# Optimization experiments

Hardware: AMD Instinct MI355X
Metric: run time of the kernel (lower is better)

## Reference

```python
import jax, jax.numpy as jnp
import numpy as np

B, L, D, H, DF = 256, 96, 512, 8, 2048
HD = D // H
SCALE = HD ** (-0.5)  # scale param (lsa=False -> constant)
EPS = 1e-5


def layer_norm(x, g, b):
    m = jnp.mean(x, axis=-1, keepdims=True)
    v = jnp.mean((x - m) ** 2, axis=-1, keepdims=True)
    return (x - m) * jax.lax.rsqrt(v + EPS) * g + b


def setup_inputs() -> dict:
    key = jax.random.key(0)
    ks = jax.random.split(key, 16)
    w = lambda k, shape: jax.random.normal(k, shape, jnp.float32) * 0.02
    return {
        "src": jax.random.normal(ks[0], (B, L, D), jnp.float32),
        "Wq": w(ks[1], (D, D)), "bq": jnp.zeros((D,), jnp.float32),
        "Wk": w(ks[2], (D, D)), "bk": jnp.zeros((D,), jnp.float32),
        "Wv": w(ks[3], (D, D)), "bv": jnp.zeros((D,), jnp.float32),
        "matrix": jax.random.normal(ks[4], (B, H, L, L), jnp.float32),  # learned per-(batch,head) score matrix
        "Wo": w(ks[5], (D, D)), "bo": jnp.zeros((D,), jnp.float32),
        "ln1_g": jnp.ones((D,), jnp.float32), "ln1_b": jnp.zeros((D,), jnp.float32),
        "W1": w(ks[6], (D, DF)), "b1": jnp.zeros((DF,), jnp.float32),
        "W2": w(ks[7], (DF, D)), "b2": jnp.zeros((D,), jnp.float32),
        "ln2_g": jnp.ones((D,), jnp.float32), "ln2_b": jnp.zeros((D,), jnp.float32),
    }


def reference(src, Wq, bq, Wk, bk, Wv, bv, matrix, Wo, bo,
              ln1_g, ln1_b, W1, b1, W2, b2, ln2_g, ln2_b):
    # --- multi-head attention with custom elementwise score matrix (NFIC=1) ---
    q = (src @ Wq + bq).reshape(B, L, H, HD).transpose(0, 2, 1, 3)  # [B,H,L,hd]
    k = (src @ Wk + bk).reshape(B, L, H, HD).transpose(0, 2, 1, 3)
    v = (src @ Wv + bv).reshape(B, L, H, HD).transpose(0, 2, 1, 3)
    scores = jnp.einsum("bhqd,bhkd->bhqk", q, k) * matrix * SCALE  # [B,H,L,L]
    attn = jax.nn.softmax(scores, axis=-1)
    out = jnp.einsum("bhqk,bhkd->bhqd", attn, v)  # [B,H,L,hd]
    out = out.transpose(0, 2, 1, 3).reshape(B, L, D) @ Wo + bo
    # --- residual + norm (post-norm) ---
    x = layer_norm(src + out, ln1_g, ln1_b)
    # --- FFN ---
    ff = jax.nn.gelu(x @ W1 + b1, approximate=False) @ W2 + b2
    y = layer_norm(x + ff, ln2_g, ln2_b)
    return (y, scores)
```

## Files before the change

kernel.cpp:

```cpp
#include <hip/hip_runtime.h>
#include <hip/hip_bf16.h>
#include <math.h>

typedef __attribute__((ext_vector_type(8))) short short8;
typedef __attribute__((ext_vector_type(4))) float floatx4;

__device__ __forceinline__ void load_lds16(const void* g, void* l) {
  __builtin_amdgcn_global_load_lds(
      (__attribute__((address_space(1))) void*)(g),
      (__attribute__((address_space(3))) void*)(l), 16, 0, 0);
}

#define MFMA16x16x32(a, b, c) __builtin_amdgcn_mfma_f32_16x16x32_bf16((a), (b), (c), 0, 0, 0)

__device__ __forceinline__ float to_f(float x) { return x; }
__device__ __forceinline__ float to_f(__hip_bfloat16 x) { return __bfloat162float(x); }
__device__ __forceinline__ void st_val(float* p, float v) { *p = v; }
__device__ __forceinline__ void st_val(__hip_bfloat16* p, float v) { *p = __float2bfloat16(v); }

__global__ __launch_bounds__(256) void cvt_f32_bf16(const float4* __restrict__ in,
                                                    ushort* __restrict__ out) {
  int i = blockIdx.x * 256 + threadIdx.x;
  float4 v = in[i];
  ushort4 o;
  __hip_bfloat16 b0 = __float2bfloat16(v.x);
  __hip_bfloat16 b1 = __float2bfloat16(v.y);
  __hip_bfloat16 b2 = __float2bfloat16(v.z);
  __hip_bfloat16 b3 = __float2bfloat16(v.w);
  o.x = *(ushort*)&b0; o.y = *(ushort*)&b1; o.z = *(ushort*)&b2; o.w = *(ushort*)&b3;
  *(ushort4*)(out + 4 * i) = o;
}

__global__ void concat3(const float* __restrict__ a, const float* __restrict__ b,
                        const float* __restrict__ c, float* __restrict__ o) {
  int i = blockIdx.x * 256 + threadIdx.x;
  o[i] = i < 512 ? a[i] : (i < 1024 ? b[i - 512] : c[i - 1024]);
}

__global__ void transpose_cvt(const float* __restrict__ in,
                              __hip_bfloat16* __restrict__ out, int R, int C) {
  __shared__ __hip_bfloat16 tile[32][33];
  int bx = blockIdx.x * 32, by = blockIdx.y * 32;
  int tx = threadIdx.x, ty = threadIdx.y;
  for (int i = ty; i < 32; i += 8)
    tile[i][tx] = __float2bfloat16(in[(size_t)(by + i) * C + bx + tx]);
  __syncthreads();
  for (int i = ty; i < 32; i += 8) out[(size_t)(bx + i) * R + by + tx] = tile[tx][i];
}

__global__ __launch_bounds__(256, 3) void gemm128(
    const __hip_bfloat16* __restrict__ A,
    const __hip_bfloat16* __restrict__ BT,
    const float* __restrict__ bias,
    __hip_bfloat16* __restrict__ C,
    int N, int K, int act, int tiles_x) {
  __shared__ __align__(16) short8 smv[2048];
  char* smc = (char*)smv;
  const int tid = threadIdx.x;
  const int wave = tid >> 6, lane = tid & 63;
  const int quad = lane >> 4, m = lane & 15;
  const int wmi = wave >> 1, wni = wave & 1;
  const int nwg = gridDim.x;
  const int wg = (blockIdx.x & 7) * (nwg >> 3) + (blockIdx.x >> 3);
  const int row0 = (wg / tiles_x) * 128;
  const int col0 = (wg % tiles_x) * 128;
  const int nt = K >> 6;

  const int colb = (((lane & 7) ^ (lane >> 3)) << 4);
  const int rbase = wave * 8 + (lane >> 3);
  const char* pA[4];
  const char* pB[4];
  char* dA[4];
  char* dB[4];
#pragma unroll
  for (int r = 0; r < 4; ++r) {
    pA[r] = (const char*)(A + (size_t)(row0 + rbase + r * 32) * K) + colb;
    pB[r] = (const char*)(BT + (size_t)(col0 + rbase + r * 32) * K) + colb;
    dA[r] = smc + (r * 4 + wave) * 1024;
    dB[r] = smc + 16384 + (r * 4 + wave) * 1024;
  }

  const int rc0 = m * 8 + ((quad)     ^ (m & 7));
  const int rc1 = m * 8 + ((quad + 4) ^ (m & 7));
  const int aB = wmi * 512;
  const int bB = 1024 + wni * 512;

  floatx4 acc[4][4] = {};

  for (int t = 0; t < nt; ++t) {
#pragma unroll
    for (int r = 0; r < 4; ++r) { load_lds16(pA[r], dA[r]); pA[r] += 128; }
#pragma unroll
    for (int r = 0; r < 4; ++r) { load_lds16(pB[r], dB[r]); pB[r] += 128; }
    __syncthreads();
    short8 aF[4], bF[4];
#pragma unroll
    for (int i = 0; i < 4; ++i) aF[i] = smv[aB + i * 128 + rc0];
#pragma unroll
    for (int j = 0; j < 4; ++j) bF[j] = smv[bB + j * 128 + rc0];
#pragma unroll
    for (int i = 0; i < 4; ++i)
#pragma unroll
      for (int j = 0; j < 4; ++j) acc[i][j] = MFMA16x16x32(aF[i], bF[j], acc[i][j]);
#pragma unroll
    for (int i = 0; i < 4; ++i) aF[i] = smv[aB + i * 128 + rc1];
#pragma unroll
    for (int j = 0; j < 4; ++j) bF[j] = smv[bB + j * 128 + rc1];
#pragma unroll
    for (int i = 0; i < 4; ++i)
#pragma unroll
      for (int j = 0; j < 4; ++j) acc[i][j] = MFMA16x16x32(aF[i], bF[j], acc[i][j]);
    __syncthreads();
  }

#pragma unroll
  for (int j = 0; j < 4; ++j) {
    const int col = col0 + wni * 64 + j * 16 + m;
    const float bj = bias[col];
#pragma unroll
    for (int i = 0; i < 4; ++i) {
      const int rowb = row0 + wmi * 64 + i * 16 + quad * 4;
#pragma unroll
      for (int r = 0; r < 4; ++r) {
        float v = acc[i][j][r] + bj;
        if (act == 1) {
          float tt = 0.7978845608f * (v + 0.044715f * v * v * v);
          float e2 = __expf(-2.0f * fabsf(tt));
          float th = (1.0f - e2) / (1.0f + e2);
          th = tt < 0.0f ? -th : th;
          v = 0.5f * v * (1.0f + th);
        }
        C[(size_t)(rowb + r) * N + col] = __float2bfloat16(v);
      }
    }
  }
}

__global__ __launch_bounds__(384) void attn_fused(
    const __hip_bfloat16* __restrict__ qkv,
    const float* __restrict__ mat,
    float* __restrict__ scores,
    __hip_bfloat16* __restrict__ ctx) {
  __shared__ __align__(16) __hip_bfloat16 Ks[96 * 72];
  __shared__ __align__(16) __hip_bfloat16 Vt[64 * 104];
  __shared__ __align__(16) __hip_bfloat16 Ps[96 * 104];
  const int bh = blockIdx.x;
  const int b = bh >> 3, h = bh & 7;
  const __hip_bfloat16* qb = qkv + (size_t)b * 96 * 1536 + h * 64;
  const __hip_bfloat16* kb = qb + 512;
  const __hip_bfloat16* vb = qb + 1024;
  const int tid = threadIdx.x;

  for (int c = tid; c < 768; c += 384) {
    int row = c >> 3, c8 = (c & 7) * 8;
    *(short8*)&Ks[row * 72 + c8] = *(const short8*)(kb + (size_t)row * 1536 + c8);
  }
  {
    int d = tid & 63;
    for (int l = tid >> 6; l < 96; l += 6) Vt[d * 104 + l] = vb[(size_t)l * 1536 + d];
  }
  __syncthreads();

  const int wave = tid >> 6, lane = tid & 63;
  const int quad = lane >> 4, m = lane & 15;

  short8 a0 = *(const short8*)(qb + (size_t)(wave * 16 + m) * 1536 + quad * 8);
  short8 a1 = *(const short8*)(qb + (size_t)(wave * 16 + m) * 1536 + 32 + quad * 8);
  floatx4 s[6];
  const size_t mbase = ((size_t)bh * 96 + wave * 16 + quad * 4) * 96 + m;
#pragma unroll
  for (int ct = 0; ct < 6; ++ct) {
    short8 b0 = *(const short8*)&Ks[(ct * 16 + m) * 72 + quad * 8];
    short8 b1 = *(const short8*)&Ks[(ct * 16 + m) * 72 + 32 + quad * 8];
    floatx4 accv = {};
    accv = MFMA16x16x32(a0, b0, accv);
    accv = MFMA16x16x32(a1, b1, accv);
#pragma unroll
    for (int r = 0; r < 4; ++r) {
      float sv = accv[r] * 0.125f * mat[mbase + (size_t)r * 96 + ct * 16];
      accv[r] = sv;
      scores[mbase + (size_t)r * 96 + ct * 16] = sv;
    }
    s[ct] = accv;
  }

#pragma unroll
  for (int r = 0; r < 4; ++r) {
    float mx = s[0][r];
#pragma unroll
    for (int ct = 1; ct < 6; ++ct) mx = fmaxf(mx, s[ct][r]);
#pragma unroll
    for (int dd = 1; dd < 16; dd <<= 1) mx = fmaxf(mx, __shfl_xor(mx, dd, 64));
    float sum = 0.f;
#pragma unroll
    for (int ct = 0; ct < 6; ++ct) {
      float e = __expf(s[ct][r] - mx);
      s[ct][r] = e;
      sum += e;
    }
#pragma unroll
    for (int dd = 1; dd < 16; dd <<= 1) sum += __shfl_xor(sum, dd, 64);
    float inv = 1.0f / sum;
#pragma unroll
    for (int ct = 0; ct < 6; ++ct)
      Ps[(wave * 16 + quad * 4 + r) * 104 + ct * 16 + m] = __float2bfloat16(s[ct][r] * inv);
  }
  __syncthreads();

  floatx4 o[4] = {};
#pragma unroll
  for (int ks = 0; ks < 3; ++ks) {
    short8 pa = *(const short8*)&Ps[(wave * 16 + m) * 104 + ks * 32 + quad * 8];
#pragma unroll
    for (int ct = 0; ct < 4; ++ct) {
      short8 vv = *(const short8*)&Vt[(ct * 16 + m) * 104 + ks * 32 + quad * 8];
      o[ct] = MFMA16x16x32(pa, vv, o[ct]);
    }
  }
  __hip_bfloat16* cb = ctx + (size_t)b * 96 * 512 + h * 64;
#pragma unroll
  for (int ct = 0; ct < 4; ++ct)
#pragma unroll
    for (int r = 0; r < 4; ++r)
      cb[(size_t)(wave * 16 + quad * 4 + r) * 512 + ct * 16 + m] = __float2bfloat16(o[ct][r]);
}

template <typename RT, typename OT>
__global__ __launch_bounds__(256) void ln_res(
    const __hip_bfloat16* __restrict__ a, const RT* __restrict__ rsd,
    const float* __restrict__ g, const float* __restrict__ be,
    OT* __restrict__ out) {
  const int row = blockIdx.x;
  const int tid = threadIdx.x;
  const size_t base = (size_t)row * 512 + tid * 2;
  float x0 = __bfloat162float(a[base]) + to_f(rsd[base]);
  float x1 = __bfloat162float(a[base + 1]) + to_f(rsd[base + 1]);
  float s = x0 + x1, s2 = x0 * x0 + x1 * x1;
#pragma unroll
  for (int d = 1; d < 64; d <<= 1) {
    s += __shfl_xor(s, d, 64);
    s2 += __shfl_xor(s2, d, 64);
  }
  __shared__ float red[8];
  const int wave = tid >> 6, lane = tid & 63;
  if (lane == 0) {
    red[wave] = s;
    red[4 + wave] = s2;
  }
  __syncthreads();
  s = red[0] + red[1] + red[2] + red[3];
  s2 = red[4] + red[5] + red[6] + red[7];
  const float mean = s * (1.0f / 512.0f);
  const float var = s2 * (1.0f / 512.0f) - mean * mean;
  const float rstd = rsqrtf(var + 1e-5f);
  st_val(out + base, (x0 - mean) * rstd * g[tid * 2] + be[tid * 2]);
  st_val(out + base + 1, (x1 - mean) * rstd * g[tid * 2 + 1] + be[tid * 2 + 1]);
}

extern "C" void kernel_launch(void* const* d_in, const int* in_sizes, int n_in,
                              void* d_out, int out_size, void* d_ws, size_t ws_size,
                              hipStream_t stream) {
  (void)in_sizes; (void)n_in; (void)out_size; (void)ws_size;
  typedef const float* cf;
  typedef __hip_bfloat16* bf;
  cf src = (cf)d_in[0];
  cf Wq = (cf)d_in[1];  cf bq = (cf)d_in[2];
  cf Wk = (cf)d_in[3];  cf bk = (cf)d_in[4];
  cf Wv = (cf)d_in[5];  cf bv = (cf)d_in[6];
  cf mat = (cf)d_in[7];
  cf Wo = (cf)d_in[8];  cf bo = (cf)d_in[9];
  cf g1 = (cf)d_in[10]; cf be1 = (cf)d_in[11];
  cf W1 = (cf)d_in[12]; cf b1 = (cf)d_in[13];
  cf W2 = (cf)d_in[14]; cf b2 = (cf)d_in[15];
  cf g2 = (cf)d_in[16]; cf be2 = (cf)d_in[17];

  char* ws = (char*)d_ws;
  const size_t SZ = (size_t)24576 * 512 * 2;
  bf qkv = (bf)(ws);
  bf ctx = (bf)(ws + 3 * SZ);
  bf hb  = (bf)(ws);
  bf srcb = (bf)(ws + 4 * SZ);
  bf tmp = (bf)(ws + 4 * SZ);
  bf xb  = (bf)(ws + 5 * SZ);
  char* wt = ws + 6 * SZ;
  bf WqkvT = (bf)(wt);
  bf WoT = (bf)(wt + 1572864);
  bf W1T = (bf)(wt + 1572864 + 524288);
  bf W2T = (bf)(wt + 1572864 + 524288 + 2097152);
  float* bqkv = (float*)(wt + 1572864 + 524288 + 2097152 + 2097152);

  float* yout = (float*)d_out;
  float* scout = (float*)d_out + 12582912;

  cvt_f32_bf16<<<12288, 256, 0, stream>>>((const float4*)src, (ushort*)srcb);
  concat3<<<6, 256, 0, stream>>>(bq, bk, bv, bqkv);

  dim3 tb(32, 8);
  transpose_cvt<<<dim3(16, 16), tb, 0, stream>>>(Wq, WqkvT, 512, 512);
  transpose_cvt<<<dim3(16, 16), tb, 0, stream>>>(Wk, WqkvT + 512 * 512, 512, 512);
  transpose_cvt<<<dim3(16, 16), tb, 0, stream>>>(Wv, WqkvT + 1024 * 512, 512, 512);
  transpose_cvt<<<dim3(16, 16), tb, 0, stream>>>(Wo, WoT, 512, 512);
  transpose_cvt<<<dim3(64, 16), tb, 0, stream>>>(W1, W1T, 512, 2048);
  transpose_cvt<<<dim3(16, 64), tb, 0, stream>>>(W2, W2T, 2048, 512);

  gemm128<<<2304, 256, 0, stream>>>(srcb, WqkvT, bqkv, qkv, 1536, 512, 0, 12);

  attn_fused<<<2048, 384, 0, stream>>>(qkv, mat, scout, ctx);

  gemm128<<<768, 256, 0, stream>>>(ctx, WoT, bo, tmp, 512, 512, 0, 4);
  ln_res<float, __hip_bfloat16><<<24576, 256, 0, stream>>>(tmp, src, g1, be1, xb);
  gemm128<<<3072, 256, 0, stream>>>(xb, W1T, b1, hb, 2048, 512, 1, 16);
  gemm128<<<768, 256, 0, stream>>>(hb, W2T, b2, tmp, 512, 2048, 0, 4);
  ln_res<__hip_bfloat16, float><<<24576, 256, 0, stream>>>(tmp, xb, g2, be2, yout);
}
```

Measured before the change: 551.8 us.

## Stage GEMM epilogue through LDS for vector stores; one-wave-per-row LayerNorm

```diff
diff --git a/kernel.cpp b/kernel.cpp
--- a/kernel.cpp
+++ b/kernel.cpp
@@ -15,8 +15,35 @@
 
 __device__ __forceinline__ float to_f(float x) { return x; }
 __device__ __forceinline__ float to_f(__hip_bfloat16 x) { return __bfloat162float(x); }
-__device__ __forceinline__ void st_val(float* p, float v) { *p = v; }
-__device__ __forceinline__ void st_val(__hip_bfloat16* p, float v) { *p = __float2bfloat16(v); }
+
+__device__ __forceinline__ void load8f(const float* p, float* x) {
+  float4 a = *(const float4*)p, b = *(const float4*)(p + 4);
+  x[0] = a.x; x[1] = a.y; x[2] = a.z; x[3] = a.w;
+  x[4] = b.x; x[5] = b.y; x[6] = b.z; x[7] = b.w;
+}
+__device__ __forceinline__ void load8f(const __hip_bfloat16* p, float* x) {
+  short8 v = *(const short8*)p;
+#pragma unroll
+  for (int k = 0; k < 8; ++k) {
+    ushort u = (ushort)v[k];
+    __hip_bfloat16 h;
+    *(ushort*)&h = u;
+    x[k] = __bfloat162float(h);
+  }
+}
+__device__ __forceinline__ void store8f(float* p, const float* x) {
+  *(float4*)p = make_float4(x[0], x[1], x[2], x[3]);
+  *(float4*)(p + 4) = make_float4(x[4], x[5], x[6], x[7]);
+}
+__device__ __forceinline__ void store8f(__hip_bfloat16* p, const float* x) {
+  short8 o;
+#pragma unroll
+  for (int k = 0; k < 8; ++k) {
+    __hip_bfloat16 h = __float2bfloat16(x[k]);
+    o[k] = *(ushort*)&h;
+  }
+  *(short8*)p = o;
+}
 
 __global__ __launch_bounds__(256) void cvt_f32_bf16(const float4* __restrict__ in,
                                                     ushort* __restrict__ out) {
@@ -48,7 +75,7 @@
   for (int i = ty; i < 32; i += 8) out[(size_t)(bx + i) * R + by + tx] = tile[tx][i];
 }
 
-__global__ __launch_bounds__(256, 3) void gemm128(
+__global__ __launch_bounds__(256, 4) void gemm128(
     const __hip_bfloat16* __restrict__ A,
     const __hip_bfloat16* __restrict__ BT,
     const float* __restrict__ bias,
@@ -113,25 +140,40 @@
     __syncthreads();
   }
 
-#pragma unroll
-  for (int j = 0; j < 4; ++j) {
-    const int col = col0 + wni * 64 + j * 16 + m;
-    const float bj = bias[col];
-#pragma unroll
-    for (int i = 0; i < 4; ++i) {
-      const int rowb = row0 + wmi * 64 + i * 16 + quad * 4;
-#pragma unroll
-      for (int r = 0; r < 4; ++r) {
-        float v = acc[i][j][r] + bj;
-        if (act == 1) {
-          float tt = 0.7978845608f * (v + 0.044715f * v * v * v);
-          float e2 = __expf(-2.0f * fabsf(tt));
-          float th = (1.0f - e2) / (1.0f + e2);
-          th = tt < 0.0f ? -th : th;
-          v = 0.5f * v * (1.0f + th);
+  {
+    ushort* se = (ushort*)smv;
+#pragma unroll
+    for (int j = 0; j < 4; ++j) {
+      const int colL = wni * 64 + j * 16 + m;
+      const float bj = bias[col0 + colL];
+#pragma unroll
+      for (int i = 0; i < 4; ++i) {
+        const int rowL = wmi * 64 + i * 16 + quad * 4;
+#pragma unroll
+        for (int r = 0; r < 4; ++r) {
+          float v = acc[i][j][r] + bj;
+          if (act == 1) {
+            float tt = 0.7978845608f * (v + 0.044715f * v * v * v);
+            float e2 = __expf(-2.0f * fabsf(tt));
+            float th = (1.0f - e2) / (1.0f + e2);
+            th = tt < 0.0f ? -th : th;
+            v = 0.5f * v * (1.0f + th);
+          }
+          const int rL = rowL + r;
+          const int byte = rL * 256 + ((colL * 2) ^ ((rL & 15) << 4));
+          __hip_bfloat16 bv = __float2bfloat16(v);
+          se[byte >> 1] = *(ushort*)&bv;
         }
-        C[(size_t)(rowb + r) * N + col] = __float2bfloat16(v);
       }
+    }
+    __syncthreads();
+#pragma unroll
+    for (int p = 0; p < 8; ++p) {
+      const int rL = p * 16 + (tid >> 4);
+      const int c = tid & 15;
+      const int byte = rL * 256 + ((c * 16) ^ ((rL & 15) << 4));
+      *(short8*)(C + (size_t)(row0 + rL) * N + col0 + c * 8) =
+          *(const short8*)(smc + byte);
     }
   }
 }
@@ -230,31 +272,33 @@
     const __hip_bfloat16* __restrict__ a, const RT* __restrict__ rsd,
     const float* __restrict__ g, const float* __restrict__ be,
     OT* __restrict__ out) {
-  const int row = blockIdx.x;
-  const int tid = threadIdx.x;
-  const size_t base = (size_t)row * 512 + tid * 2;
-  float x0 = __bfloat162float(a[base]) + to_f(rsd[base]);
-  float x1 = __bfloat162float(a[base + 1]) + to_f(rsd[base + 1]);
-  float s = x0 + x1, s2 = x0 * x0 + x1 * x1;
+  const int row = blockIdx.x * 4 + (threadIdx.x >> 6);
+  const int lane = threadIdx.x & 63;
+  const size_t base = (size_t)row * 512 + lane * 8;
+  float x[8], rv[8];
+  load8f(a + base, x);
+  load8f(rsd + base, rv);
+  float s = 0.f, s2 = 0.f;
+#pragma unroll
+  for (int k = 0; k < 8; ++k) {
+    x[k] += rv[k];
+    s += x[k];
+    s2 += x[k] * x[k];
+  }
 #pragma unroll
   for (int d = 1; d < 64; d <<= 1) {
     s += __shfl_xor(s, d, 64);
     s2 += __shfl_xor(s2, d, 64);
   }
-  __shared__ float red[8];
-  const int wave = tid >> 6, lane = tid & 63;
-  if (lane == 0) {
-    red[wave] = s;
-    red[4 + wave] = s2;
-  }
-  __syncthreads();
-  s = red[0] + red[1] + red[2] + red[3];
-  s2 = red[4] + red[5] + red[6] + red[7];
   const float mean = s * (1.0f / 512.0f);
   const float var = s2 * (1.0f / 512.0f) - mean * mean;
   const float rstd = rsqrtf(var + 1e-5f);
-  st_val(out + base, (x0 - mean) * rstd * g[tid * 2] + be[tid * 2]);
-  st_val(out + base + 1, (x1 - mean) * rstd * g[tid * 2 + 1] + be[tid * 2 + 1]);
+  float gv[8], bv[8], y[8];
+  load8f(g + lane * 8, gv);
+  load8f(be + lane * 8, bv);
+#pragma unroll
+  for (int k = 0; k < 8; ++k) y[k] = (x[k] - mean) * rstd * gv[k] + bv[k];
+  store8f(out + base, y);
 }
 
 extern "C" void kernel_launch(void* const* d_in, const int* in_sizes, int n_in,
@@ -308,8 +352,8 @@
   attn_fused<<<2048, 384, 0, stream>>>(qkv, mat, scout, ctx);
 
   gemm128<<<768, 256, 0, stream>>>(ctx, WoT, bo, tmp, 512, 512, 0, 4);
-  ln_res<float, __hip_bfloat16><<<24576, 256, 0, stream>>>(tmp, src, g1, be1, xb);
+  ln_res<float, __hip_bfloat16><<<6144, 256, 0, stream>>>(tmp, src, g1, be1, xb);
   gemm128<<<3072, 256, 0, stream>>>(xb, W1T, b1, hb, 2048, 512, 1, 16);
   gemm128<<<768, 256, 0, stream>>>(hb, W2T, b2, tmp, 512, 2048, 0, 4);
-  ln_res<__hip_bfloat16, float><<<24576, 256, 0, stream>>>(tmp, xb, g2, be2, yout);
-}
+  ln_res<__hip_bfloat16, float><<<6144, 256, 0, stream>>>(tmp, xb, g2, be2, yout);
+}
```

Measured after the change: 536.3 us. 1.03x faster.
